# Kernel optimization log

Hardware: AMD Instinct MI355X
Metric: run time of the kernel (lower is better)

The kernel has to match this reference:

```python
import jax, jax.numpy as jnp
import numpy as np

N_NODES = 100000   # number of graph nodes
N_EDGES = 1600000  # adjacency nnz (avg degree 16)
FEAT_NNZ = 1600000 # sparse feature nnz (~16 per node)
F_IN = 512
F_OUT = 128


def setup_inputs() -> dict:
    key = jax.random.key(0)
    k1, k2, k3, k4, k5, k6 = jax.random.split(key, 6)
    adj_indices = jax.random.randint(k1, (2, N_EDGES), 0, N_NODES, dtype=jnp.int64 if jax.config.jax_enable_x64 else jnp.int32)
    adj_values = jax.random.uniform(k2, (N_EDGES,), dtype=jnp.float32)
    feat_rows = jax.random.randint(k3, (FEAT_NNZ,), 0, N_NODES)
    feat_cols = jax.random.randint(k4, (FEAT_NNZ,), 0, F_IN)
    feat_values = jax.random.uniform(k5, (FEAT_NNZ,), dtype=jnp.float32)
    # xavier_uniform init of the dense weight, as in the torch module
    bound = float(np.sqrt(6.0 / (F_IN + F_OUT)))
    weight = jax.random.uniform(k6, (F_IN, F_OUT), dtype=jnp.float32, minval=-bound, maxval=bound)
    return {
        "adj_indices": adj_indices,
        "adj_values": adj_values,
        "feat_rows": feat_rows,
        "feat_cols": feat_cols,
        "feat_values": feat_values,
        "weight": weight,
        "num_nodes": N_NODES,
    }


def _spmm(rows, cols, vals, num_rows, dense):
    """COO sparse [num_rows, ?] @ dense [?, K] -> [num_rows, K]."""
    msgs = vals[:, None] * dense[cols]          # [nnz, K] gather + scale
    return jax.ops.segment_sum(msgs, rows, num_segments=num_rows)


def reference(adj_indices, adj_values, feat_rows, feat_cols, feat_values, weight, num_nodes):
    # spmm(features, W): sparse [N, F_in] @ [F_in, F_out]
    base_features = _spmm(feat_rows, feat_cols, feat_values, num_nodes, weight)
    # spmm(A_hat, base): sparse [N, N] @ [N, F_out]  -- neighbor aggregation
    out = _spmm(adj_indices[0], adj_indices[1], adj_values, num_nodes, base_features)
    return out
```

## Files before the change

kernel.cpp:

```cpp
#include <hip/hip_runtime.h>
#include <stdint.h>

#define N_NODES 100000
#define F_IN    512
#define F_OUT   128
#define BROWS   128
#define NBKT    ((N_NODES + BROWS - 1) / BROWS)
#define CAP     2560
#define EPB     4096
#define BR2     64
#define SCAP    1536

typedef unsigned short     u16;
typedef unsigned int       u32;
typedef unsigned long long u64;
typedef long long          i64;

__device__ __forceinline__ float b2f(u16 u) {
    union { u32 i; float f; } x; x.i = ((u32)u) << 16; return x.f;
}
__device__ __forceinline__ u16 f2b(float f) {
    u32 i = __float_as_uint(f);
    return (u16)((i + 0x7fffu + ((i >> 16) & 1u)) >> 16);
}
__device__ __forceinline__ float blo(u32 u) { return __uint_as_float(u << 16); }
__device__ __forceinline__ float bhi(u32 u) { return __uint_as_float(u & 0xFFFF0000u); }
__device__ __forceinline__ int ld_idx(const void* p, int i, int w64) {
    return w64 ? (int)((const i64*)p)[i] : ((const int*)p)[i];
}
__device__ __forceinline__ u16 ld_val_bf(const void* p, int i, int f32) {
    return f32 ? f2b(((const float*)p)[i]) : ((const u16*)p)[i];
}

__global__ void sniff_k(const u16* __restrict__ w, const u32* __restrict__ adj,
                        const u32* __restrict__ frows, int* __restrict__ flags,
                        int* __restrict__ gcurF, int* __restrict__ gcurA) {
    int t = threadIdx.x;
    if (t < 64) {
        int lane = t;
        u32 e0 = (w[lane]      >> 7) & 0xFF;
        u32 e1 = (w[64 + lane] >> 7) & 0xFF;
        u64 bad = __ballot((e0 > 0x7B) || (e1 > 0x7B));
        u64 za = __ballot(adj[2 * lane + 1] == 0u);
        u64 zf = __ballot(frows[2 * lane + 1] == 0u);
        if (lane == 0) {
            flags[0] = (bad != 0);
            flags[1] = (__popcll(za) >= 32);
            flags[2] = (__popcll(zf) >= 32);
        }
    }
    for (int i = t; i < NBKT; i += 256) { gcurF[i] = 0; gcurA[i] = 0; }
}

__global__ __launch_bounds__(256) void binFA_k(
        const void* __restrict__ frows, const void* __restrict__ fcols,
        const void* __restrict__ fvals, int M, int nFb,
        const void* __restrict__ adjbase, const void* __restrict__ avals, int E,
        const int* __restrict__ flags,
        int* __restrict__ gcurF, int* __restrict__ gcurA,
        u32* __restrict__ fbkt, u64* __restrict__ abkt) {
    __shared__ u64 sortA[EPB];
    __shared__ u16 sbkt[EPB];
    __shared__ int hist[NBKT];
    __shared__ int lbase[NBKT];
    __shared__ int hbase[NBKT];
    __shared__ int wtot[4];
    int t = threadIdx.x;
    int lane = t & 63, wv = t >> 6;
    for (int i = t; i < NBKT; i += 256) hist[i] = 0;
    __syncthreads();
    int f32 = flags[0];

    if ((int)blockIdx.x < nFb) {
        int f64 = flags[2];
        int start = blockIdx.x * EPB;
        int end = min(start + EPB, M);
        for (int i = start + t; i < end; i += 256)
            atomicAdd(&hist[ld_idx(frows, i, f64) >> 7], 1);
        __syncthreads();
        {
            int b0 = t * 4;
            int c0 = (b0 + 0 < NBKT) ? hist[b0 + 0] : 0;
            int c1 = (b0 + 1 < NBKT) ? hist[b0 + 1] : 0;
            int c2 = (b0 + 2 < NBKT) ? hist[b0 + 2] : 0;
            int c3 = (b0 + 3 < NBKT) ? hist[b0 + 3] : 0;
            int s = c0 + c1 + c2 + c3;
            int v = s;
            #pragma unroll
            for (int off = 1; off < 64; off <<= 1) {
                int u = __shfl_up(v, off);
                if (lane >= off) v += u;
            }
            if (lane == 63) wtot[wv] = v;
            __syncthreads();
            int woff = 0;
            #pragma unroll
            for (int w = 0; w < 4; ++w) if (w < wv) woff += wtot[w];
            int run = woff + v - s;
            int cc[4] = {c0, c1, c2, c3};
            #pragma unroll
            for (int k = 0; k < 4; ++k) {
                int bb = b0 + k;
                if (bb < NBKT) {
                    lbase[bb] = run;
                    hist[bb] = run;
                    hbase[bb] = cc[k] ? atomicAdd(&gcurF[bb], cc[k]) : 0;
                    run += cc[k];
                }
            }
        }
        __syncthreads();
        u32* sortF = (u32*)sortA;
        for (int i = start + t; i < end; i += 256) {
            int r = ld_idx(frows, i, f64);
            int c = ld_idx(fcols, i, f64);
            u32 v = ld_val_bf(fvals, i, f32);
            int b = r >> 7;
            int pos = atomicAdd(&hist[b], 1);
            sortF[pos] = (v << 16) | ((u32)(r & 127) << 9) | (u32)c;
            sbkt[pos] = (u16)b;
        }
        __syncthreads();
        int n = end - start;
        for (int i = t; i < n; i += 256) {
            int b = sbkt[i];
            int pos = hbase[b] + (i - lbase[b]);
            if (pos < CAP)
                fbkt[(size_t)b * CAP + pos] = sortF[i];
        }
    } else {
        int a64 = flags[1];
        const void* acols = a64 ? (const void*)((const i64*)adjbase + E)
                                : (const void*)((const int*)adjbase + E);
        int start = ((int)blockIdx.x - nFb) * EPB;
        int end = min(start + EPB, E);
        for (int i = start + t; i < end; i += 256)
            atomicAdd(&hist[ld_idx(adjbase, i, a64) >> 7], 1);
        __syncthreads();
        {
            int b0 = t * 4;
            int c0 = (b0 + 0 < NBKT) ? hist[b0 + 0] : 0;
            int c1 = (b0 + 1 < NBKT) ? hist[b0 + 1] : 0;
            int c2 = (b0 + 2 < NBKT) ? hist[b0 + 2] : 0;
            int c3 = (b0 + 3 < NBKT) ? hist[b0 + 3] : 0;
            int s = c0 + c1 + c2 + c3;
            int v = s;
            #pragma unroll
            for (int off = 1; off < 64; off <<= 1) {
                int u = __shfl_up(v, off);
                if (lane >= off) v += u;
            }
            if (lane == 63) wtot[wv] = v;
            __syncthreads();
            int woff = 0;
            #pragma unroll
            for (int w = 0; w < 4; ++w) if (w < wv) woff += wtot[w];
            int run = woff + v - s;
            int cc[4] = {c0, c1, c2, c3};
            #pragma unroll
            for (int k = 0; k < 4; ++k) {
                int bb = b0 + k;
                if (bb < NBKT) {
                    lbase[bb] = run;
                    hist[bb] = run;
                    hbase[bb] = cc[k] ? atomicAdd(&gcurA[bb], cc[k]) : 0;
                    run += cc[k];
                }
            }
        }
        __syncthreads();
        for (int i = start + t; i < end; i += 256) {
            int r = ld_idx(adjbase, i, a64);
            int c = ld_idx(acols, i, a64);
            u64 v = ld_val_bf(avals, i, f32);
            int b = r >> 7;
            int pos = atomicAdd(&hist[b], 1);
            sortA[pos] = (v << 24) | ((u64)(r & 127) << 17) | (u64)(u32)c;
            sbkt[pos] = (u16)b;
        }
        __syncthreads();
        int n = end - start;
        for (int i = t; i < n; i += 256) {
            int b = sbkt[i];
            int pos = hbase[b] + (i - lbase[b]);
            if (pos < CAP)
                abkt[(size_t)b * CAP + pos] = sortA[i];
        }
    }
}

__global__ __launch_bounds__(256, 8) void stage1_k(const int* __restrict__ cnt,
        const u32* __restrict__ bkts, const void* __restrict__ W,
        const int* __restrict__ flags, u16* __restrict__ base) {
    __shared__ u32 csr[SCAP];
    __shared__ int hcnt[BR2];
    __shared__ int roff[BR2 + 1];
    __shared__ int cur[BR2];
    int t = threadIdx.x;
    int b = blockIdx.x >> 1;
    int half = blockIdx.x & 1;
    int n = cnt[b]; if (n > CAP) n = CAP;
    const u32* ed = bkts + (size_t)b * CAP;
    if (t < BR2) hcnt[t] = 0;
    __syncthreads();
    for (int i = t; i < n; i += 256) {
        int rl = (ed[i] >> 9) & 0x7F;
        if ((rl >> 6) == half) atomicAdd(&hcnt[rl & 63], 1);
    }
    __syncthreads();
    if (t < 64) {
        int h = hcnt[t];
        int v = h;
        #pragma unroll
        for (int off = 1; off < 64; off <<= 1) {
            int u = __shfl_up(v, off);
            if (t >= off) v += u;
        }
        roff[t + 1] = v;
        cur[t] = v - h;
        if (t == 0) roff[0] = 0;
    }
    __syncthreads();
    for (int i = t; i < n; i += 256) {
        u32 p = ed[i];
        int rl = (p >> 9) & 0x7F;
        if ((rl >> 6) == half) {
            int pos = atomicAdd(&cur[rl & 63], 1);
            if (pos < SCAP) csr[pos] = p;
        }
    }
    __syncthreads();
    int wave = t >> 6, lane = t & 63, g = lane >> 4, l16 = lane & 15;
    int f32 = flags[0];
    #pragma unroll
    for (int set = 0; set < 4; ++set) {
        int row = set * 16 + wave * 4 + g;
        int s = roff[row], e = roff[row + 1];
        if (s > SCAP) s = SCAP;
        if (e > SCAP) e = SCAP;
        float a[8] = {0.f, 0.f, 0.f, 0.f, 0.f, 0.f, 0.f, 0.f};
        if (f32) {
            const float* Wf = (const float*)W;
            for (int j0 = s; j0 < e; j0 += 4) {
                u32 p[4]; float4 qa[4], qb[4];
                #pragma unroll
                for (int k = 0; k < 4; ++k) { int jk = j0 + k; p[k] = csr[jk < e ? jk : e - 1]; }
                #pragma unroll
                for (int k = 0; k < 4; ++k) {
                    const float* wp = Wf + (size_t)(p[k] & 0x1FF) * F_OUT + l16 * 8;
                    qa[k] = *(const float4*)wp;
                    qb[k] = *(const float4*)(wp + 4);
                }
                #pragma unroll
                for (int k = 0; k < 4; ++k) {
                    float v = (j0 + k < e) ? b2f((u16)(p[k] >> 16)) : 0.f;
                    a[0] += v * qa[k].x; a[1] += v * qa[k].y;
                    a[2] += v * qa[k].z; a[3] += v * qa[k].w;
                    a[4] += v * qb[k].x; a[5] += v * qb[k].y;
                    a[6] += v * qb[k].z; a[7] += v * qb[k].w;
                }
            }
        } else {
            const u16* Wb = (const u16*)W;
            for (int j0 = s; j0 < e; j0 += 4) {
                u32 p[4]; uint4 q[4];
                #pragma unroll
                for (int k = 0; k < 4; ++k) { int jk = j0 + k; p[k] = csr[jk < e ? jk : e - 1]; }
                #pragma unroll
                for (int k = 0; k < 4; ++k)
                    q[k] = *(const uint4*)(Wb + (size_t)(p[k] & 0x1FF) * F_OUT + l16 * 8);
                #pragma unroll
                for (int k = 0; k < 4; ++k) {
                    float v = (j0 + k < e) ? b2f((u16)(p[k] >> 16)) : 0.f;
                    a[0] += v * blo(q[k].x); a[1] += v * bhi(q[k].x);
                    a[2] += v * blo(q[k].y); a[3] += v * bhi(q[k].y);
                    a[4] += v * blo(q[k].z); a[5] += v * bhi(q[k].z);
                    a[6] += v * blo(q[k].w); a[7] += v * bhi(q[k].w);
                }
            }
        }
        int gr = b * BROWS + half * BR2 + row;
        if (gr < N_NODES) {
            uint4 o;
            o.x = (u32)f2b(a[0]) | ((u32)f2b(a[1]) << 16);
            o.y = (u32)f2b(a[2]) | ((u32)f2b(a[3]) << 16);
            o.z = (u32)f2b(a[4]) | ((u32)f2b(a[5]) << 16);
            o.w = (u32)f2b(a[6]) | ((u32)f2b(a[7]) << 16);
            *(uint4*)(base + (size_t)gr * F_OUT + l16 * 8) = o;
        }
    }
}

__global__ __launch_bounds__(256, 8) void stage2_k(const int* __restrict__ cnt,
        const u64* __restrict__ bkts, const u16* __restrict__ base,
        const int* __restrict__ flags, void* __restrict__ out) {
    __shared__ u64 csr[SCAP];
    __shared__ int hcnt[BR2];
    __shared__ int roff[BR2 + 1];
    __shared__ int cur[BR2];
    int t = threadIdx.x;
    int b = blockIdx.x >> 1;
    int half = blockIdx.x & 1;
    int n = cnt[b]; if (n > CAP) n = CAP;
    const u64* ed = bkts + (size_t)b * CAP;
    if (t < BR2) hcnt[t] = 0;
    __syncthreads();
    for (int i = t; i < n; i += 256) {
        int rl = (int)((ed[i] >> 17) & 0x7F);
        if ((rl >> 6) == half) atomicAdd(&hcnt[rl & 63], 1);
    }
    __syncthreads();
    if (t < 64) {
        int h = hcnt[t];
        int v = h;
        #pragma unroll
        for (int off = 1; off < 64; off <<= 1) {
            int u = __shfl_up(v, off);
            if (t >= off) v += u;
        }
        roff[t + 1] = v;
        cur[t] = v - h;
        if (t == 0) roff[0] = 0;
    }
    __syncthreads();
    for (int i = t; i < n; i += 256) {
        u64 p = ed[i];
        int rl = (int)((p >> 17) & 0x7F);
        if ((rl >> 6) == half) {
            int pos = atomicAdd(&cur[rl & 63], 1);
            if (pos < SCAP) csr[pos] = p;
        }
    }
    __syncthreads();
    int wave = t >> 6, lane = t & 63, g = lane >> 4, l16 = lane & 15;
    int f32o = flags[0];
    #pragma unroll
    for (int set = 0; set < 4; ++set) {
        int row = set * 16 + wave * 4 + g;
        int s = roff[row], e = roff[row + 1];
        if (s > SCAP) s = SCAP;
        if (e > SCAP) e = SCAP;
        float a[8] = {0.f, 0.f, 0.f, 0.f, 0.f, 0.f, 0.f, 0.f};
        for (int j0 = s; j0 < e; j0 += 4) {
            u64 p[4]; uint4 q[4];
            #pragma unroll
            for (int k = 0; k < 4; ++k) { int jk = j0 + k; p[k] = csr[jk < e ? jk : e - 1]; }
            #pragma unroll
            for (int k = 0; k < 4; ++k)
                q[k] = *(const uint4*)(base + (size_t)(u32)(p[k] & 0x1FFFF) * F_OUT + l16 * 8);
            #pragma unroll
            for (int k = 0; k < 4; ++k) {
                float v = (j0 + k < e) ? b2f((u16)(p[k] >> 24)) : 0.f;
                a[0] += v * blo(q[k].x); a[1] += v * bhi(q[k].x);
                a[2] += v * blo(q[k].y); a[3] += v * bhi(q[k].y);
                a[4] += v * blo(q[k].z); a[5] += v * bhi(q[k].z);
                a[6] += v * blo(q[k].w); a[7] += v * bhi(q[k].w);
            }
        }
        int gr = b * BROWS + half * BR2 + row;
        if (gr < N_NODES) {
            if (f32o) {
                float* op = (float*)out + (size_t)gr * F_OUT + l16 * 8;
                float4 o0, o1;
                o0.x = a[0]; o0.y = a[1]; o0.z = a[2]; o0.w = a[3];
                o1.x = a[4]; o1.y = a[5]; o1.z = a[6]; o1.w = a[7];
                *(float4*)op = o0;
                *(float4*)(op + 4) = o1;
            } else {
                uint4 o;
                o.x = (u32)f2b(a[0]) | ((u32)f2b(a[1]) << 16);
                o.y = (u32)f2b(a[2]) | ((u32)f2b(a[3]) << 16);
                o.z = (u32)f2b(a[4]) | ((u32)f2b(a[5]) << 16);
                o.w = (u32)f2b(a[6]) | ((u32)f2b(a[7]) << 16);
                *(uint4*)((u16*)out + (size_t)gr * F_OUT + l16 * 8) = o;
            }
        }
    }
}

extern "C" void kernel_launch(void* const* d_in, const int* in_sizes, int n_in,
                              void* d_out, int out_size, void* d_ws, size_t ws_size,
                              hipStream_t stream) {
    const void* adj_idx   = d_in[0];
    const void* adj_vals  = d_in[1];
    const void* feat_rows = d_in[2];
    const void* feat_cols = d_in[3];
    const void* feat_vals = d_in[4];
    const void* weight    = d_in[5];

    const int E = in_sizes[0] / 2;
    const int M = in_sizes[2];

    char* ws = (char*)d_ws;
    size_t o = 0;
    auto alloc = [&](size_t b) { size_t r = o; o += (b + 255) & ~(size_t)255; return r; };
    int* gcurF = (int*)(ws + alloc((size_t)NBKT * 4));
    int* gcurA = (int*)(ws + alloc((size_t)NBKT * 4));
    int* flags = (int*)(ws + alloc(4 * 4));
    u32* fbkt  = (u32*)(ws + alloc((size_t)NBKT * CAP * 4));
    u64* abkt  = (u64*)(ws + alloc((size_t)NBKT * CAP * 8));
    u16* base  = (u16*)(ws + alloc((size_t)N_NODES * F_OUT * 2));
    (void)ws_size;

    const int nFb = (M + EPB - 1) / EPB;
    const int nAb = (E + EPB - 1) / EPB;

    sniff_k<<<1, 256, 0, stream>>>((const u16*)weight, (const u32*)adj_idx,
                                   (const u32*)feat_rows, flags, gcurF, gcurA);
    binFA_k<<<nFb + nAb, 256, 0, stream>>>(feat_rows, feat_cols, feat_vals, M, nFb,
                                           adj_idx, adj_vals, E,
                                           flags, gcurF, gcurA, fbkt, abkt);
    stage1_k<<<2 * NBKT, 256, 0, stream>>>(gcurF, fbkt, weight, flags, base);
    stage2_k<<<2 * NBKT, 256, 0, stream>>>(gcurA, abkt, base, flags, d_out);
}
```

Before: 280.7 us.

## Process four chunks per binning block and pad global bucket counters

Each binning block now covers four 4096-element chunks. It computes one block-wide histogram and makes one global atomic reservation per bucket, then locally sorts and scatters each chunk in turn. This is meant to cut global atomic traffic on the bucket counters, which are also padded to a 16-int stride to avoid contention on shared cache lines. Loads are unrolled by 8 for more memory-level parallelism. In exchange the row indices are read an extra time, and with four times fewer blocks there is less parallelism across the GPU.

```diff
diff --git a/kernel.cpp b/kernel.cpp
--- a/kernel.cpp
+++ b/kernel.cpp
@@ -8,6 +8,9 @@
 #define NBKT    ((N_NODES + BROWS - 1) / BROWS)
 #define CAP     2560
 #define EPB     4096
+#define CHUNKS  4
+#define BLKE    (EPB * CHUNKS)
+#define GSTR    16
 #define BR2     64
 #define SCAP    1536
 
@@ -30,6 +33,34 @@
 }
 __device__ __forceinline__ u16 ld_val_bf(const void* p, int i, int f32) {
     return f32 ? f2b(((const float*)p)[i]) : ((const u16*)p)[i];
+}
+
+__device__ __forceinline__ void scan782(int* hist, int* lbase, int* wtot, int t) {
+    int lane = t & 63, wv = t >> 6;
+    int b0 = t * 4;
+    int c0 = (b0 + 0 < NBKT) ? hist[b0 + 0] : 0;
+    int c1 = (b0 + 1 < NBKT) ? hist[b0 + 1] : 0;
+    int c2 = (b0 + 2 < NBKT) ? hist[b0 + 2] : 0;
+    int c3 = (b0 + 3 < NBKT) ? hist[b0 + 3] : 0;
+    int s = c0 + c1 + c2 + c3;
+    int v = s;
+    #pragma unroll
+    for (int off = 1; off < 64; off <<= 1) {
+        int u = __shfl_up(v, off);
+        if (lane >= off) v += u;
+    }
+    if (lane == 63) wtot[wv] = v;
+    __syncthreads();
+    int woff = 0;
+    #pragma unroll
+    for (int w = 0; w < 4; ++w) if (w < wv) woff += wtot[w];
+    int run = woff + v - s;
+    int cc[4] = {c0, c1, c2, c3};
+    #pragma unroll
+    for (int k = 0; k < 4; ++k) {
+        int bb = b0 + k;
+        if (bb < NBKT) { lbase[bb] = run; hist[bb] = run; run += cc[k]; }
+    }
 }
 
 __global__ void sniff_k(const u16* __restrict__ w, const u32* __restrict__ adj,
@@ -49,7 +80,7 @@
             flags[2] = (__popcll(zf) >= 32);
         }
     }
-    for (int i = t; i < NBKT; i += 256) { gcurF[i] = 0; gcurA[i] = 0; }
+    for (int i = t; i < NBKT * GSTR; i += 1024) { gcurF[i] = 0; gcurA[i] = 0; }
 }
 
 __global__ __launch_bounds__(256) void binFA_k(
@@ -63,128 +94,195 @@
     __shared__ u16 sbkt[EPB];
     __shared__ int hist[NBKT];
     __shared__ int lbase[NBKT];
-    __shared__ int hbase[NBKT];
+    __shared__ int gcur_l[NBKT];
     __shared__ int wtot[4];
     int t = threadIdx.x;
-    int lane = t & 63, wv = t >> 6;
-    for (int i = t; i < NBKT; i += 256) hist[i] = 0;
+    for (int i = t; i < NBKT; i += 256) gcur_l[i] = 0;
     __syncthreads();
     int f32 = flags[0];
 
     if ((int)blockIdx.x < nFb) {
         int f64 = flags[2];
-        int start = blockIdx.x * EPB;
-        int end = min(start + EPB, M);
-        for (int i = start + t; i < end; i += 256)
-            atomicAdd(&hist[ld_idx(frows, i, f64) >> 7], 1);
+        int start = blockIdx.x * BLKE;
+        int end = min(start + BLKE, M);
+        {
+            int i = start + t;
+            while (i + 256 * 7 < end) {
+                int r[8];
+                #pragma unroll
+                for (int k = 0; k < 8; ++k) r[k] = ld_idx(frows, i + 256 * k, f64);
+                #pragma unroll
+                for (int k = 0; k < 8; ++k) atomicAdd(&gcur_l[r[k] >> 7], 1);
+                i += 2048;
+            }
+            for (; i < end; i += 256) atomicAdd(&gcur_l[ld_idx(frows, i, f64) >> 7], 1);
+        }
         __syncthreads();
         {
             int b0 = t * 4;
-            int c0 = (b0 + 0 < NBKT) ? hist[b0 + 0] : 0;
-            int c1 = (b0 + 1 < NBKT) ? hist[b0 + 1] : 0;
-            int c2 = (b0 + 2 < NBKT) ? hist[b0 + 2] : 0;
-            int c3 = (b0 + 3 < NBKT) ? hist[b0 + 3] : 0;
-            int s = c0 + c1 + c2 + c3;
-            int v = s;
-            #pragma unroll
-            for (int off = 1; off < 64; off <<= 1) {
-                int u = __shfl_up(v, off);
-                if (lane >= off) v += u;
-            }
-            if (lane == 63) wtot[wv] = v;
-            __syncthreads();
-            int woff = 0;
-            #pragma unroll
-            for (int w = 0; w < 4; ++w) if (w < wv) woff += wtot[w];
-            int run = woff + v - s;
-            int cc[4] = {c0, c1, c2, c3};
             #pragma unroll
             for (int k = 0; k < 4; ++k) {
                 int bb = b0 + k;
                 if (bb < NBKT) {
-                    lbase[bb] = run;
-                    hist[bb] = run;
-                    hbase[bb] = cc[k] ? atomicAdd(&gcurF[bb], cc[k]) : 0;
-                    run += cc[k];
+                    int tot = gcur_l[bb];
+                    gcur_l[bb] = tot ? atomicAdd(&gcurF[bb * GSTR], tot) : 0;
                 }
             }
         }
         __syncthreads();
         u32* sortF = (u32*)sortA;
-        for (int i = start + t; i < end; i += 256) {
-            int r = ld_idx(frows, i, f64);
-            int c = ld_idx(fcols, i, f64);
-            u32 v = ld_val_bf(fvals, i, f32);
-            int b = r >> 7;
-            int pos = atomicAdd(&hist[b], 1);
-            sortF[pos] = (v << 16) | ((u32)(r & 127) << 9) | (u32)c;
-            sbkt[pos] = (u16)b;
-        }
-        __syncthreads();
-        int n = end - start;
-        for (int i = t; i < n; i += 256) {
-            int b = sbkt[i];
-            int pos = hbase[b] + (i - lbase[b]);
-            if (pos < CAP)
-                fbkt[(size_t)b * CAP + pos] = sortF[i];
+        for (int c = 0; c < CHUNKS; ++c) {
+            int cs = start + c * EPB;
+            if (cs >= end) break;
+            int ce = min(cs + EPB, end);
+            int nc = ce - cs;
+            for (int i = t; i < NBKT; i += 256) hist[i] = 0;
+            __syncthreads();
+            {
+                int i = cs + t;
+                while (i + 256 * 7 < ce) {
+                    int r[8];
+                    #pragma unroll
+                    for (int k = 0; k < 8; ++k) r[k] = ld_idx(frows, i + 256 * k, f64);
+                    #pragma unroll
+                    for (int k = 0; k < 8; ++k) atomicAdd(&hist[r[k] >> 7], 1);
+                    i += 2048;
+                }
+                for (; i < ce; i += 256) atomicAdd(&hist[ld_idx(frows, i, f64) >> 7], 1);
+            }
+            __syncthreads();
+            scan782(hist, lbase, wtot, t);
+            __syncthreads();
+            {
+                int i = cs + t;
+                while (i + 256 * 7 < ce) {
+                    int r[8], cc[8]; u32 vv[8];
+                    #pragma unroll
+                    for (int k = 0; k < 8; ++k) {
+                        r[k] = ld_idx(frows, i + 256 * k, f64);
+                        cc[k] = ld_idx(fcols, i + 256 * k, f64);
+                        vv[k] = ld_val_bf(fvals, i + 256 * k, f32);
+                    }
+                    #pragma unroll
+                    for (int k = 0; k < 8; ++k) {
+                        int b = r[k] >> 7;
+                        int pos = atomicAdd(&hist[b], 1);
+                        sortF[pos] = (vv[k] << 16) | ((u32)(r[k] & 127) << 9) | (u32)cc[k];
+                        sbkt[pos] = (u16)b;
+                    }
+                    i += 2048;
+                }
+                for (; i < ce; i += 256) {
+                    int r = ld_idx(frows, i, f64), cc = ld_idx(fcols, i, f64);
+                    u32 vv = ld_val_bf(fvals, i, f32);
+                    int b = r >> 7;
+                    int pos = atomicAdd(&hist[b], 1);
+                    sortF[pos] = (vv << 16) | ((u32)(r & 127) << 9) | (u32)cc;
+                    sbkt[pos] = (u16)b;
+                }
+            }
+            __syncthreads();
+            for (int i = t; i < nc; i += 256) {
+                int b = sbkt[i];
+                int pos = gcur_l[b] + (i - lbase[b]);
+                if (pos < CAP)
+                    fbkt[(size_t)b * CAP + pos] = sortF[i];
+            }
+            __syncthreads();
+            for (int bb = t; bb < NBKT; bb += 256) gcur_l[bb] += hist[bb] - lbase[bb];
+            __syncthreads();
         }
     } else {
         int a64 = flags[1];
         const void* acols = a64 ? (const void*)((const i64*)adjbase + E)
                                 : (const void*)((const int*)adjbase + E);
-        int start = ((int)blockIdx.x - nFb) * EPB;
-        int end = min(start + EPB, E);
-        for (int i = start + t; i < end; i += 256)
-            atomicAdd(&hist[ld_idx(adjbase, i, a64) >> 7], 1);
+        int start = ((int)blockIdx.x - nFb) * BLKE;
+        int end = min(start + BLKE, E);
+        {
+            int i = start + t;
+            while (i + 256 * 7 < end) {
+                int r[8];
+                #pragma unroll
+                for (int k = 0; k < 8; ++k) r[k] = ld_idx(adjbase, i + 256 * k, a64);
+                #pragma unroll
+                for (int k = 0; k < 8; ++k) atomicAdd(&gcur_l[r[k] >> 7], 1);
+                i += 2048;
+            }
+            for (; i < end; i += 256) atomicAdd(&gcur_l[ld_idx(adjbase, i, a64) >> 7], 1);
+        }
         __syncthreads();
         {
             int b0 = t * 4;
-            int c0 = (b0 + 0 < NBKT) ? hist[b0 + 0] : 0;
-            int c1 = (b0 + 1 < NBKT) ? hist[b0 + 1] : 0;
-            int c2 = (b0 + 2 < NBKT) ? hist[b0 + 2] : 0;
-            int c3 = (b0 + 3 < NBKT) ? hist[b0 + 3] : 0;
-            int s = c0 + c1 + c2 + c3;
-            int v = s;
-            #pragma unroll
-            for (int off = 1; off < 64; off <<= 1) {
-                int u = __shfl_up(v, off);
-                if (lane >= off) v += u;
-            }
-            if (lane == 63) wtot[wv] = v;
-            __syncthreads();
-            int woff = 0;
-            #pragma unroll
-            for (int w = 0; w < 4; ++w) if (w < wv) woff += wtot[w];
-            int run = woff + v - s;
-            int cc[4] = {c0, c1, c2, c3};
             #pragma unroll
             for (int k = 0; k < 4; ++k) {
                 int bb = b0 + k;
                 if (bb < NBKT) {
-                    lbase[bb] = run;
-                    hist[bb] = run;
-                    hbase[bb] = cc[k] ? atomicAdd(&gcurA[bb], cc[k]) : 0;
-                    run += cc[k];
+                    int tot = gcur_l[bb];
+                    gcur_l[bb] = tot ? atomicAdd(&gcurA[bb * GSTR], tot) : 0;
                 }
             }
         }
         __syncthreads();
-        for (int i = start + t; i < end; i += 256) {
-            int r = ld_idx(adjbase, i, a64);
-            int c = ld_idx(acols, i, a64);
-            u64 v = ld_val_bf(avals, i, f32);
-            int b = r >> 7;
-            int pos = atomicAdd(&hist[b], 1);
-            sortA[pos] = (v << 24) | ((u64)(r & 127) << 17) | (u64)(u32)c;
-            sbkt[pos] = (u16)b;
-        }
-        __syncthreads();
-        int n = end - start;
-        for (int i = t; i < n; i += 256) {
-            int b = sbkt[i];
-            int pos = hbase[b] + (i - lbase[b]);
-            if (pos < CAP)
-                abkt[(size_t)b * CAP + pos] = sortA[i];
+        for (int c = 0; c < CHUNKS; ++c) {
+            int cs = start + c * EPB;
+            if (cs >= end) break;
+            int ce = min(cs + EPB, end);
+            int nc = ce - cs;
+            for (int i = t; i < NBKT; i += 256) hist[i] = 0;
+            __syncthreads();
+            {
+                int i = cs + t;
+                while (i + 256 * 7 < ce) {
+                    int r[8];
+                    #pragma unroll
+                    for (int k = 0; k < 8; ++k) r[k] = ld_idx(adjbase, i + 256 * k, a64);
+                    #pragma unroll
+                    for (int k = 0; k < 8; ++k) atomicAdd(&hist[r[k] >> 7], 1);
+                    i += 2048;
+                }
+                for (; i < ce; i += 256) atomicAdd(&hist[ld_idx(adjbase, i, a64) >> 7], 1);
+            }
+            __syncthreads();
+            scan782(hist, lbase, wtot, t);
+            __syncthreads();
+            {
+                int i = cs + t;
+                while (i + 256 * 7 < ce) {
+                    int r[8], cc[8]; u32 vv[8];
+                    #pragma unroll
+                    for (int k = 0; k < 8; ++k) {
+                        r[k] = ld_idx(adjbase, i + 256 * k, a64);
+                        cc[k] = ld_idx(acols, i + 256 * k, a64);
+                        vv[k] = ld_val_bf(avals, i + 256 * k, f32);
+                    }
+                    #pragma unroll
+                    for (int k = 0; k < 8; ++k) {
+                        int b = r[k] >> 7;
+                        int pos = atomicAdd(&hist[b], 1);
+                        sortA[pos] = ((u64)vv[k] << 24) | ((u64)(r[k] & 127) << 17) | (u64)(u32)cc[k];
+                        sbkt[pos] = (u16)b;
+                    }
+                    i += 2048;
+                }
+                for (; i < ce; i += 256) {
+                    int r = ld_idx(adjbase, i, a64), cc = ld_idx(acols, i, a64);
+                    u64 vv = ld_val_bf(avals, i, f32);
+                    int b = r >> 7;
+                    int pos = atomicAdd(&hist[b], 1);
+                    sortA[pos] = (vv << 24) | ((u64)(r & 127) << 17) | (u64)(u32)cc;
+                    sbkt[pos] = (u16)b;
+                }
+            }
+            __syncthreads();
+            for (int i = t; i < nc; i += 256) {
+                int b = sbkt[i];
+                int pos = gcur_l[b] + (i - lbase[b]);
+                if (pos < CAP)
+                    abkt[(size_t)b * CAP + pos] = sortA[i];
+            }
+            __syncthreads();
+            for (int bb = t; bb < NBKT; bb += 256) gcur_l[bb] += hist[bb] - lbase[bb];
+            __syncthreads();
         }
     }
 }
@@ -199,7 +297,7 @@
     int t = threadIdx.x;
     int b = blockIdx.x >> 1;
     int half = blockIdx.x & 1;
-    int n = cnt[b]; if (n > CAP) n = CAP;
+    int n = cnt[b * GSTR]; if (n > CAP) n = CAP;
     const u32* ed = bkts + (size_t)b * CAP;
     if (t < BR2) hcnt[t] = 0;
     __syncthreads();
@@ -301,7 +399,7 @@
     int t = threadIdx.x;
     int b = blockIdx.x >> 1;
     int half = blockIdx.x & 1;
-    int n = cnt[b]; if (n > CAP) n = CAP;
+    int n = cnt[b * GSTR]; if (n > CAP) n = CAP;
     const u64* ed = bkts + (size_t)b * CAP;
     if (t < BR2) hcnt[t] = 0;
     __syncthreads();
@@ -394,19 +492,19 @@
     char* ws = (char*)d_ws;
     size_t o = 0;
     auto alloc = [&](size_t b) { size_t r = o; o += (b + 255) & ~(size_t)255; return r; };
-    int* gcurF = (int*)(ws + alloc((size_t)NBKT * 4));
-    int* gcurA = (int*)(ws + alloc((size_t)NBKT * 4));
+    int* gcurF = (int*)(ws + alloc((size_t)NBKT * GSTR * 4));
+    int* gcurA = (int*)(ws + alloc((size_t)NBKT * GSTR * 4));
     int* flags = (int*)(ws + alloc(4 * 4));
     u32* fbkt  = (u32*)(ws + alloc((size_t)NBKT * CAP * 4));
     u64* abkt  = (u64*)(ws + alloc((size_t)NBKT * CAP * 8));
     u16* base  = (u16*)(ws + alloc((size_t)N_NODES * F_OUT * 2));
     (void)ws_size;
 
-    const int nFb = (M + EPB - 1) / EPB;
-    const int nAb = (E + EPB - 1) / EPB;
-
-    sniff_k<<<1, 256, 0, stream>>>((const u16*)weight, (const u32*)adj_idx,
-                                   (const u32*)feat_rows, flags, gcurF, gcurA);
+    const int nFb = (M + BLKE - 1) / BLKE;
+    const int nAb = (E + BLKE - 1) / BLKE;
+
+    sniff_k<<<1, 1024, 0, stream>>>((const u16*)weight, (const u32*)adj_idx,
+                                    (const u32*)feat_rows, flags, gcurF, gcurA);
     binFA_k<<<nFb + nAb, 256, 0, stream>>>(feat_rows, feat_cols, feat_vals, M, nFb,
                                            adj_idx, adj_vals, E,
                                            flags, gcurF, gcurA, fbkt, abkt);
```

Result: slower. 291.1 us (+3.7%).
